# Kernel tuning notes

Hardware: AMD Instinct MI355X
Metric: run time of the kernel (lower is better)

## Reference

```python
import jax, jax.numpy as jnp
import numpy as np

D = 16777216  # per-feature embedding width (batch pinned to 1 by original code's view(1, len(data)))


def setup_inputs() -> dict:
    key = jax.random.key(0)
    k0, k1, k2, k3 = jax.random.split(key, 4)
    x = jax.random.normal(k0, (1, D), dtype=jnp.float32)
    ly_0 = jax.random.normal(k1, (1, D), dtype=jnp.float32)
    ly_1 = jax.random.normal(k2, (1, D), dtype=jnp.float32)
    ly_2 = jax.random.normal(k3, (1, D), dtype=jnp.float32)
    return {"x": x, "ly_0": ly_0, "ly_1": ly_1, "ly_2": ly_2}


def reference(x, ly_0, ly_1, ly_2):
    # DLRM dot-interaction: T = [B, 4, d], Z = T @ T^T -> [B, 4, 4]
    B, d = x.shape
    T = jnp.concatenate([x, ly_0, ly_1, ly_2], axis=1).reshape(B, -1, d)
    Z = jnp.einsum('bid,bjd->bij', T, T)  # [B, 4, 4]
    # strict lower-triangular gather (arch_interaction_itself=False -> offset=0)
    li, lj = np.tril_indices(T.shape[1], k=-1)  # rows [1,2,2,3,3,3], cols [0,0,1,0,1,2]
    # original torch code cats per-pair [B] slices then view(1, n_pairs) -> valid only for B=1
    Zflat = Z[:, li, lj].reshape(1, len(li))  # [1, 6]
    R = jnp.concatenate([x, Zflat], axis=1)  # [1, d + 6]
    return R
```

## Files before the change

### kernel.cpp

```cpp
#include <hip/hip_runtime.h>


typedef float fvec4 __attribute__((ext_vector_type(4)));

constexpr int D_TOTAL = 16777216;
constexpr int NVEC    = D_TOTAL / 4;
constexpr int BLOCK   = 256;
constexpr int GRID    = 2048;
constexpr int ITERS   = NVEC / (BLOCK * GRID);
static_assert(NVEC == BLOCK * GRID * ITERS, "exact tiling");

#define FMA4(acc, u, v) \
    acc += u.x * v.x + u.y * v.y + u.z * v.z + u.w * v.w;

__global__ __launch_bounds__(BLOCK) void dlrm_dot(
        const fvec4* __restrict__ x,
        const fvec4* __restrict__ l0,
        const fvec4* __restrict__ l1,
        const fvec4* __restrict__ l2,
        float* __restrict__ partials)
{
    float s[6] = {0.f, 0.f, 0.f, 0.f, 0.f, 0.f};

    const int base   = blockIdx.x * BLOCK + threadIdx.x;
    const int stride = BLOCK * GRID;

    #pragma unroll 2
    for (int it = 0; it < ITERS; ++it) {
        const int i = base + it * stride;
        const fvec4 a = x[i];
        const fvec4 b = l0[i];
        const fvec4 c = l1[i];
        const fvec4 d = l2[i];
        FMA4(s[0], a, b)
        FMA4(s[1], a, c)
        FMA4(s[2], b, c)
        FMA4(s[3], a, d)
        FMA4(s[4], b, d)
        FMA4(s[5], c, d)
    }

    #pragma unroll
    for (int off = 32; off > 0; off >>= 1) {
        #pragma unroll
        for (int k = 0; k < 6; ++k)
            s[k] += __shfl_down(s[k], off, 64);
    }

    __shared__ float red[BLOCK / 64][6];
    const int wave = threadIdx.x >> 6;
    const int lane = threadIdx.x & 63;
    if (lane == 0) {
        #pragma unroll
        for (int k = 0; k < 6; ++k) red[wave][k] = s[k];
    }
    __syncthreads();

    if (threadIdx.x < 6) {
        float tot = 0.f;
        #pragma unroll
        for (int w = 0; w < BLOCK / 64; ++w) tot += red[w][threadIdx.x];
        partials[threadIdx.x * GRID + blockIdx.x] = tot;
    }
}

__global__ __launch_bounds__(384) void dlrm_reduce(
        const float* __restrict__ partials, float* __restrict__ out_pairs)
{
    const int w    = threadIdx.x >> 6;
    const int lane = threadIdx.x & 63;
    const float* row = partials + w * GRID;
    float s = 0.f;
    #pragma unroll
    for (int i = 0; i < GRID / 64; ++i) s += row[lane + i * 64];
    #pragma unroll
    for (int off = 32; off > 0; off >>= 1) s += __shfl_down(s, off, 64);
    if (lane == 0) out_pairs[w] = s;
}

__global__ void dlrm_init_pairs(float* __restrict__ out) {
    if (threadIdx.x < 6) out[(size_t)D_TOTAL + threadIdx.x] = 0.0f;
}

__global__ __launch_bounds__(BLOCK) void dlrm_dot_atomic(
        const fvec4* __restrict__ x, const fvec4* __restrict__ l0,
        const fvec4* __restrict__ l1, const fvec4* __restrict__ l2,
        float* __restrict__ out_pairs)
{
    float s[6] = {0.f, 0.f, 0.f, 0.f, 0.f, 0.f};
    const int base = blockIdx.x * BLOCK + threadIdx.x;
    const int stride = BLOCK * GRID;
    #pragma unroll 2
    for (int it = 0; it < ITERS; ++it) {
        const int i = base + it * stride;
        const fvec4 a = x[i], b = l0[i], c = l1[i], d = l2[i];
        FMA4(s[0], a, b) FMA4(s[1], a, c) FMA4(s[2], b, c)
        FMA4(s[3], a, d) FMA4(s[4], b, d) FMA4(s[5], c, d)
    }
    #pragma unroll
    for (int off = 32; off > 0; off >>= 1)
        #pragma unroll
        for (int k = 0; k < 6; ++k) s[k] += __shfl_down(s[k], off, 64);
    __shared__ float red[BLOCK / 64][6];
    const int wave = threadIdx.x >> 6, lane = threadIdx.x & 63;
    if (lane == 0)
        for (int k = 0; k < 6; ++k) red[wave][k] = s[k];
    __syncthreads();
    if (threadIdx.x < 6) {
        float tot = 0.f;
        for (int w = 0; w < BLOCK / 64; ++w) tot += red[w][threadIdx.x];
        atomicAdd(out_pairs + threadIdx.x, tot);
    }
}

extern "C" void kernel_launch(void* const* d_in, const int* in_sizes, int n_in,
                              void* d_out, int out_size, void* d_ws, size_t ws_size,
                              hipStream_t stream) {
    const fvec4* x  = (const fvec4*)d_in[0];
    const fvec4* l0 = (const fvec4*)d_in[1];
    const fvec4* l1 = (const fvec4*)d_in[2];
    const fvec4* l2 = (const fvec4*)d_in[3];
    float* out = (float*)d_out;

    if (ws_size >= (size_t)6 * GRID * sizeof(float)) {
        float* partials = (float*)d_ws;
        dlrm_dot<<<GRID, BLOCK, 0, stream>>>(x, l0, l1, l2, partials);
        dlrm_reduce<<<1, 384, 0, stream>>>(partials, out + (size_t)D_TOTAL);
    } else {
        dlrm_init_pairs<<<1, 64, 0, stream>>>(out);
        dlrm_dot_atomic<<<GRID, BLOCK, 0, stream>>>(
            x, l0, l1, l2, out + (size_t)D_TOTAL);
    }
    hipMemcpyAsync(out, x, (size_t)D_TOTAL * sizeof(float),
                   hipMemcpyDeviceToDevice, stream);
}
```

Measured before the change: 273.7 us.

## Fuse output copy of x into dot-interaction kernel with nontemporal stores

The separate device-to-device memcpy of x into the output is removed. Each thread now writes the x vector it already loaded with a nontemporal store, which saves a full re-read of x and one extra operation on the stream. The access pattern also changes from a grid-strided loop to a contiguous chunk per block, with deeper unrolling. The risk is that a per-block contiguous layout changes how memory channels are spread and adds write traffic inside the compute kernel.

```diff
diff --git a/kernel.cpp b/kernel.cpp
--- a/kernel.cpp
+++ b/kernel.cpp
@@ -7,31 +7,33 @@
 constexpr int NVEC    = D_TOTAL / 4;
 constexpr int BLOCK   = 256;
 constexpr int GRID    = 2048;
-constexpr int ITERS   = NVEC / (BLOCK * GRID);
-static_assert(NVEC == BLOCK * GRID * ITERS, "exact tiling");
+constexpr int CHUNK   = NVEC / GRID;
+constexpr int ITERS   = CHUNK / BLOCK;
+static_assert(NVEC == GRID * CHUNK && CHUNK == BLOCK * ITERS, "exact tiling");
 
 #define FMA4(acc, u, v) \
     acc += u.x * v.x + u.y * v.y + u.z * v.z + u.w * v.w;
 
-__global__ __launch_bounds__(BLOCK) void dlrm_dot(
+__global__ __launch_bounds__(BLOCK) void dlrm_interact_main(
         const fvec4* __restrict__ x,
         const fvec4* __restrict__ l0,
         const fvec4* __restrict__ l1,
         const fvec4* __restrict__ l2,
+        fvec4* __restrict__ out_copy,
         float* __restrict__ partials)
 {
     float s[6] = {0.f, 0.f, 0.f, 0.f, 0.f, 0.f};
 
-    const int base   = blockIdx.x * BLOCK + threadIdx.x;
-    const int stride = BLOCK * GRID;
+    const int base = blockIdx.x * CHUNK + threadIdx.x;
 
-    #pragma unroll 2
+    #pragma unroll 4
     for (int it = 0; it < ITERS; ++it) {
-        const int i = base + it * stride;
+        const int i = base + it * BLOCK;
         const fvec4 a = x[i];
         const fvec4 b = l0[i];
         const fvec4 c = l1[i];
         const fvec4 d = l2[i];
+        __builtin_nontemporal_store(a, &out_copy[i]);
         FMA4(s[0], a, b)
         FMA4(s[1], a, c)
         FMA4(s[2], b, c)
@@ -82,18 +84,18 @@
     if (threadIdx.x < 6) out[(size_t)D_TOTAL + threadIdx.x] = 0.0f;
 }
 
-__global__ __launch_bounds__(BLOCK) void dlrm_dot_atomic(
+__global__ __launch_bounds__(BLOCK) void dlrm_interact_atomic(
         const fvec4* __restrict__ x, const fvec4* __restrict__ l0,
         const fvec4* __restrict__ l1, const fvec4* __restrict__ l2,
-        float* __restrict__ out_pairs)
+        fvec4* __restrict__ out_copy, float* __restrict__ out_pairs)
 {
     float s[6] = {0.f, 0.f, 0.f, 0.f, 0.f, 0.f};
-    const int base = blockIdx.x * BLOCK + threadIdx.x;
-    const int stride = BLOCK * GRID;
-    #pragma unroll 2
+    const int base = blockIdx.x * CHUNK + threadIdx.x;
+    #pragma unroll 4
     for (int it = 0; it < ITERS; ++it) {
-        const int i = base + it * stride;
+        const int i = base + it * BLOCK;
         const fvec4 a = x[i], b = l0[i], c = l1[i], d = l2[i];
+        __builtin_nontemporal_store(a, &out_copy[i]);
         FMA4(s[0], a, b) FMA4(s[1], a, c) FMA4(s[2], b, c)
         FMA4(s[3], a, d) FMA4(s[4], b, d) FMA4(s[5], c, d)
     }
@@ -124,13 +126,12 @@
 
     if (ws_size >= (size_t)6 * GRID * sizeof(float)) {
         float* partials = (float*)d_ws;
-        dlrm_dot<<<GRID, BLOCK, 0, stream>>>(x, l0, l1, l2, partials);
+        dlrm_interact_main<<<GRID, BLOCK, 0, stream>>>(
+            x, l0, l1, l2, (fvec4*)out, partials);
         dlrm_reduce<<<1, 384, 0, stream>>>(partials, out + (size_t)D_TOTAL);
     } else {
         dlrm_init_pairs<<<1, 64, 0, stream>>>(out);
-        dlrm_dot_atomic<<<GRID, BLOCK, 0, stream>>>(
-            x, l0, l1, l2, out + (size_t)D_TOTAL);
+        dlrm_interact_atomic<<<GRID, BLOCK, 0, stream>>>(
+            x, l0, l1, l2, (fvec4*)out, out + (size_t)D_TOTAL);
     }
-    hipMemcpyAsync(out, x, (size_t)D_TOTAL * sizeof(float),
-                   hipMemcpyDeviceToDevice, stream);
 }
```

Measured after the change: 269.7 us. No clear change (-1.4%).
